# Kernel tuning notes

Measured on AMD Instinct MI355X. Metric: run time of the kernel, lower is better.

The kernel has to match this reference:

```python
import jax, jax.numpy as jnp
import numpy as np

N_HEADS = 8
EMBED_DIM = 64  # per-head dim


def setup_inputs() -> dict:
    key = jax.random.key(0)
    k1, k2, k3 = jax.random.split(key, 3)
    B, S, F = 2, 2048, 512
    x = jax.random.normal(k1, (B, S, F), dtype=jnp.float32)
    W = jax.random.normal(k2, (F, EMBED_DIM * N_HEADS * 3), dtype=jnp.float32) * 0.02
    b = jax.random.normal(k3, (EMBED_DIM * N_HEADS * 3,), dtype=jnp.float32) * 0.02
    return {"x": x, "W": W, "b": b}


def reference(x, W, b):
    B, S, F = x.shape
    H, E = N_HEADS, EMBED_DIM
    emb = x @ W + b                                   # (B, S, E*H*3)
    heads = emb.reshape(B, S, E, H, 3)
    heads = jnp.transpose(heads, (0, 4, 3, 1, 2))     # (B, 3, H, S, E)
    q, k, v = heads[:, 0], heads[:, 1], heads[:, 2]   # each (B, H, S, E)
    qk = jnp.einsum('bhse,bhte->bhst', q, k)          # (B, H, S, S)
    # Original multiplies softmax by `scaling` then divides by it -> exact cancel.
    # Note: no scaling applied BEFORE softmax in the source (faithful).
    attn = jax.nn.softmax(qk, axis=-1)
    out = jnp.einsum('bhst,bhte->bhse', attn, v)      # (B, H, S, E)
    out = jnp.transpose(out, (0, 2, 1, 3)).reshape(B, S, H * E)
    return out
```

## Files before the change

kernel.cpp:

```cpp
#include <hip/hip_runtime.h>


using half8  = __attribute__((ext_vector_type(8))) _Float16;
using f32x4  = __attribute__((ext_vector_type(4))) float;
using float4v = __attribute__((ext_vector_type(4))) float;
using uint2v = __attribute__((ext_vector_type(2))) unsigned int;
using uint4v = __attribute__((ext_vector_type(4))) unsigned int;

constexpr int BN = 2, HN = 8, SN = 2048, EN = 64, FN = 512;
constexpr size_t T_ELEMS = (size_t)BN * HN * SN * EN;

constexpr size_t WB_BYTES = (size_t)24 * 16 * 4 * 64 * 8 * 2;
constexpr size_t BP_OFF   = WB_BYTES;
constexpr size_t X16_OFF  = BP_OFF + 1536 * 4;
constexpr size_t X16_BYTES = (size_t)4096 * 512 * 2;
constexpr size_t QKV_OFF  = X16_OFF + X16_BYTES;

__device__ inline unsigned int pack2h(float a, float b) {
  auto h = __builtin_amdgcn_cvt_pkrtz(a, b);
  return __builtin_bit_cast(unsigned int, h);
}

__device__ __forceinline__ void async_copy16(void* lds, const void* g) {
  __builtin_amdgcn_global_load_lds(
      (const __attribute__((address_space(1))) unsigned int*)g,
      (__attribute__((address_space(3))) unsigned int*)lds, 16, 0, 0);
}

__global__ __launch_bounds__(256) void repack_kernel(
    const float* __restrict__ W, const float* __restrict__ bias,
    _Float16* __restrict__ Wb, float* __restrict__ bp) {
  int t = blockIdx.x * 256 + threadIdx.x;
  int lane = t & 63;
  int cb = (t >> 6) & 3;
  int kc = (t >> 8) & 15;
  int ch = t >> 12;
  int e = cb * 16 + (lane & 15);
  int fb = kc * 32 + (lane >> 4) * 8;
  int c = ch >> 3, h = ch & 7;
  int j = e * 24 + h * 3 + c;
  half8 o;
  #pragma unroll
  for (int i = 0; i < 8; ++i) o[i] = (_Float16)W[(size_t)(fb + i) * 1536 + j];
  *(half8*)(Wb + (size_t)t * 8) = o;
  if (t < 1536) {
    int cc = t % 3, hh = (t / 3) & 7, ee = t / 24;
    bp[(cc * 8 + hh) * 64 + ee] = bias[t];
  }
}

__global__ __launch_bounds__(256) void x16_kernel(const float* __restrict__ x,
                                                  _Float16* __restrict__ x16) {
  int t = blockIdx.x * 256 + threadIdx.x;
  const float4v* src = (const float4v*)(x + (size_t)t * 8);
  float4v a = src[0], b = src[1];
  half8 o;
  #pragma unroll
  for (int i = 0; i < 4; ++i) { o[i] = (_Float16)a[i]; o[4 + i] = (_Float16)b[i]; }
  *(half8*)(x16 + (size_t)t * 8) = o;
}

__global__ __launch_bounds__(256) void proj_kernel(
    const _Float16* __restrict__ x16, const _Float16* __restrict__ Wb,
    const float* __restrict__ bp, _Float16* __restrict__ qkv) {
  int rt = blockIdx.x, cg = blockIdx.y;
  int wave = threadIdx.x >> 6, lane = threadIdx.x & 63;
  int lcol = lane & 15, lg = lane >> 4;
  int row0 = rt * 64 + wave * 16;
  f32x4 acc[3][4] = {};
  const _Float16* xr = x16 + (size_t)(row0 + lcol) * FN;
  for (int kc = 0; kc < 16; ++kc) {
    half8 a = *(const half8*)(xr + kc * 32 + lg * 8);
    #pragma unroll
    for (int chi = 0; chi < 3; ++chi) {
      int ch = cg * 3 + chi;
      #pragma unroll
      for (int cb = 0; cb < 4; ++cb) {
        half8 bfr = *(const half8*)(Wb + ((((size_t)ch * 16 + kc) * 4 + cb) * 64 + lane) * 8);
        acc[chi][cb] = __builtin_amdgcn_mfma_f32_16x16x32_f16(a, bfr, acc[chi][cb], 0, 0, 0);
      }
    }
  }
  #pragma unroll
  for (int chi = 0; chi < 3; ++chi) {
    int ch = cg * 3 + chi;
    int c = ch >> 3, h = ch & 7;
    _Float16* dst = qkv + (size_t)c * T_ELEMS;
    #pragma unroll
    for (int cb = 0; cb < 4; ++cb) {
      int e = cb * 16 + lcol;
      float bv = bp[ch * 64 + e];
      #pragma unroll
      for (int r = 0; r < 4; ++r) {
        int grow = row0 + lg * 4 + r;
        int b = grow >> 11, s = grow & 2047;
        dst[((size_t)(b * HN + h) * SN + s) * EN + e] = (_Float16)(acc[chi][cb][r] + bv);
      }
    }
  }
}

__global__ __launch_bounds__(256) void vtrans_kernel(const _Float16* __restrict__ v,
                                                     _Float16* __restrict__ vt) {
  __shared__ _Float16 tl[64 * 65];
  int bh = blockIdx.x >> 5, st = blockIdx.x & 31;
  int t = threadIdx.x;
  int s0 = st * 64;
  int sl = t >> 3, e0 = (t & 7) * 8;
  #pragma unroll
  for (int rr = 0; rr < 2; ++rr) {
    half8 vv = *(const half8*)(v + ((size_t)bh * SN + s0 + sl + rr * 32) * EN + e0);
    #pragma unroll
    for (int i = 0; i < 8; ++i) tl[(sl + rr * 32) * 65 + e0 + i] = vv[i];
  }
  __syncthreads();
  int e = t >> 2, sc = t & 3;
  half8 o0, o1;
  #pragma unroll
  for (int i = 0; i < 8; ++i) o0[i] = tl[(sc * 16 + i) * 65 + e];
  #pragma unroll
  for (int i = 0; i < 8; ++i) o1[i] = tl[(sc * 16 + 8 + i) * 65 + e];
  _Float16* dst = vt + ((size_t)bh * EN + e) * SN + s0 + sc * 16;
  *(half8*)dst = o0;
  *(half8*)(dst + 8) = o1;
}

__global__ __launch_bounds__(256, 2) void attn_kernel(
    const _Float16* __restrict__ q_ws, const _Float16* __restrict__ k_ws,
    const _Float16* __restrict__ vt_ws, float* __restrict__ out) {
  __shared__ __align__(16) char smem[40960];

  int bid = blockIdx.x;
  int lb = (bid & 7) * 64 + (bid >> 3);
  int bh = lb >> 5, qblk = lb & 31;
  int wave = threadIdx.x >> 6, lane = threadIdx.x & 63;
  int q = lane & 15, g = lane >> 4;
  int q0 = qblk * 64 + wave * 16;

  const _Float16* qb  = q_ws  + ((size_t)bh * SN + q0) * EN;
  const _Float16* kb  = k_ws  + (size_t)bh * SN * EN;
  const _Float16* vtb = vt_ws + (size_t)bh * EN * SN;

  half8 qf[2];
  qf[0] = *(const half8*)(qb + (size_t)q * EN + g * 8);
  qf[1] = *(const half8*)(qb + (size_t)q * EN + 32 + g * 8);

  f32x4 o[4] = {};
  float m = -3e38f, l = 0.f;
  unsigned int* pw = (unsigned int*)(smem + 32768 + wave * 2048);

  int sub = lane >> 3;
  int off8 = ((lane & 7) ^ sub) * 8;
  int lin = lane * 16;

  auto stage = [&](int c, int t) {
    char* kbuf = smem + c * 16384;
    char* vbuf = kbuf + 8192;
    int kv = t * 64;
    #pragma unroll
    for (int ii = 0; ii < 2; ++ii) {
      int i = wave * 2 + ii;
      int row = i * 8 + sub;
      async_copy16(kbuf + i * 1024 + lin, kb + (size_t)(kv + row) * EN + off8);
      async_copy16(vbuf + i * 1024 + lin, vtb + (size_t)row * SN + kv + off8);
    }
  };

  stage(0, 0);
  asm volatile("s_waitcnt vmcnt(0)" ::: "memory");
  __syncthreads();

  int qx = (q & 7) << 4;
  for (int t = 0; t < 32; ++t) {
    int c = t & 1;
    if (t + 1 < 32) stage(c ^ 1, t + 1);
    const char* kbuf = smem + c * 16384;
    const char* vbuf = kbuf + 8192;

    half8 kf[4][2], vf[4][2];
    #pragma unroll
    for (int kt = 0; kt < 4; ++kt)
      #pragma unroll
      for (int eh = 0; eh < 2; ++eh)
        kf[kt][eh] = *(const half8*)(kbuf + ((((kt * 16 + q) * 128) + eh * 64 + g * 16) ^ qx));
    #pragma unroll
    for (int et = 0; et < 4; ++et)
      #pragma unroll
      for (int kh = 0; kh < 2; ++kh)
        vf[et][kh] = *(const half8*)(vbuf + ((((et * 16 + q) * 128) + kh * 64 + g * 16) ^ qx));

    f32x4 s[4];
    f32x4 z = {};
    __builtin_amdgcn_s_setprio(1);
    #pragma unroll
    for (int kt = 0; kt < 4; ++kt) {
      s[kt] = __builtin_amdgcn_mfma_f32_16x16x32_f16(kf[kt][0], qf[0], z, 0, 0, 0);
      s[kt] = __builtin_amdgcn_mfma_f32_16x16x32_f16(kf[kt][1], qf[1], s[kt], 0, 0, 0);
    }
    __builtin_amdgcn_s_setprio(0);

    float mx = s[0][0];
    #pragma unroll
    for (int kt = 0; kt < 4; ++kt)
      #pragma unroll
      for (int r = 0; r < 4; ++r) mx = fmaxf(mx, s[kt][r]);
    mx = fmaxf(mx, __shfl_xor(mx, 16));
    mx = fmaxf(mx, __shfl_xor(mx, 32));
    if (!__all(mx <= m + 8.f)) {
      float mn = fmaxf(m, mx);
      float scl = __expf(m - mn);
      m = mn;
      l *= scl;
      #pragma unroll
      for (int et = 0; et < 4; ++et)
        #pragma unroll
        for (int r = 0; r < 4; ++r) o[et][r] *= scl;
    }
    float ps = 0.f;
    #pragma unroll
    for (int kt = 0; kt < 4; ++kt) {
      float p0 = __expf(s[kt][0] - m), p1 = __expf(s[kt][1] - m);
      float p2 = __expf(s[kt][2] - m), p3 = __expf(s[kt][3] - m);
      ps += (p0 + p1) + (p2 + p3);
      uint2v wv;
      wv.x = pack2h(p0, p1);
      wv.y = pack2h(p2, p3);
      int w = kt * 8 + 2 * g;
      int phys = (((w >> 2) + q) & 7) * 4 + (w & 3);
      *(uint2v*)&pw[q * 32 + phys] = wv;
    }
    l += ps;
    asm volatile("s_waitcnt lgkmcnt(0)" ::: "memory");
    __builtin_amdgcn_sched_barrier(0);
    half8 pf[2];
    #pragma unroll
    for (int kh = 0; kh < 2; ++kh) {
      int cc = kh * 4 + g;
      uint4v tv = *(const uint4v*)&pw[q * 32 + ((cc + q) & 7) * 4];
      pf[kh] = __builtin_bit_cast(half8, tv);
    }
    __builtin_amdgcn_sched_barrier(0);
    __builtin_amdgcn_s_setprio(1);
    #pragma unroll
    for (int et = 0; et < 4; ++et) {
      o[et] = __builtin_amdgcn_mfma_f32_16x16x32_f16(vf[et][0], pf[0], o[et], 0, 0, 0);
      o[et] = __builtin_amdgcn_mfma_f32_16x16x32_f16(vf[et][1], pf[1], o[et], 0, 0, 0);
    }
    __builtin_amdgcn_s_setprio(0);

    asm volatile("s_waitcnt vmcnt(0)" ::: "memory");
    __syncthreads();
  }

  l += __shfl_xor(l, 16);
  l += __shfl_xor(l, 32);
  float rl = 1.f / l;
  int b = bh >> 3, h = bh & 7;
  float* ow = (float*)(smem + wave * 4096);
  #pragma unroll
  for (int et = 0; et < 4; ++et)
    #pragma unroll
    for (int r = 0; r < 4; ++r) {
      int e = et * 16 + g * 4 + r;
      ow[q * 64 + ((e + q * 4) & 63)] = o[et][r] * rl;
    }
  asm volatile("s_waitcnt lgkmcnt(0)" ::: "memory");
  __builtin_amdgcn_sched_barrier(0);
  #pragma unroll
  for (int qr = 0; qr < 16; ++qr) {
    float vvv = ow[qr * 64 + ((lane + qr * 4) & 63)];
    out[((size_t)b * SN + q0 + qr) * 512 + h * 64 + lane] = vvv;
  }
}

extern "C" void kernel_launch(void* const* d_in, const int* in_sizes, int n_in,
                              void* d_out, int out_size, void* d_ws, size_t ws_size,
                              hipStream_t stream) {
  const float* x    = (const float*)d_in[0];
  const float* W    = (const float*)d_in[1];
  const float* bias = (const float*)d_in[2];
  float* out = (float*)d_out;
  char* ws = (char*)d_ws;
  _Float16* Wb  = (_Float16*)(ws);
  float*    bp  = (float*)(ws + BP_OFF);
  _Float16* x16 = (_Float16*)(ws + X16_OFF);
  _Float16* qkv = (_Float16*)(ws + QKV_OFF);
  _Float16* vt  = (_Float16*)(ws + X16_OFF);

  repack_kernel<<<384, 256, 0, stream>>>(W, bias, Wb, bp);
  x16_kernel<<<1024, 256, 0, stream>>>(x, x16);
  proj_kernel<<<dim3(64, 8), 256, 0, stream>>>(x16, Wb, bp, qkv);
  vtrans_kernel<<<512, 256, 0, stream>>>(qkv + 2 * T_ELEMS, vt);
  attn_kernel<<<512, 256, 0, stream>>>(qkv, qkv + T_ELEMS, vt, out);
}
```

Baseline: 130.9 us.

## Fuse x conversion and V transpose into projection; triple-buffer attention K/V

The separate fp32→fp16 conversion kernel for x is removed; the projection kernel now loads fp32 x and converts in registers. The V transpose kernel is also folded into the projection epilogue, which transposes V through shared memory and writes Vt directly. The attention kernel moves from double to triple buffering of K/V tiles, issuing loads two tiles ahead with a partial vmcnt wait, which raises LDS use to 56KB per block. Together these remove two kernel launches and their extra global round-trips, and deepen the load prefetch, at the cost of larger fp32 reads in projection and more LDS pressure in attention.

```diff
diff --git a/kernel.cpp b/kernel.cpp
--- a/kernel.cpp
+++ b/kernel.cpp
@@ -12,9 +12,9 @@
 
 constexpr size_t WB_BYTES = (size_t)24 * 16 * 4 * 64 * 8 * 2;
 constexpr size_t BP_OFF   = WB_BYTES;
-constexpr size_t X16_OFF  = BP_OFF + 1536 * 4;
-constexpr size_t X16_BYTES = (size_t)4096 * 512 * 2;
-constexpr size_t QKV_OFF  = X16_OFF + X16_BYTES;
+constexpr size_t VT_OFF   = BP_OFF + 1536 * 4;
+constexpr size_t VT_BYTES = T_ELEMS * 2;
+constexpr size_t QKV_OFF  = VT_OFF + VT_BYTES;
 
 __device__ inline unsigned int pack2h(float a, float b) {
   auto h = __builtin_amdgcn_cvt_pkrtz(a, b);
@@ -49,28 +49,23 @@
   }
 }
 
-__global__ __launch_bounds__(256) void x16_kernel(const float* __restrict__ x,
-                                                  _Float16* __restrict__ x16) {
-  int t = blockIdx.x * 256 + threadIdx.x;
-  const float4v* src = (const float4v*)(x + (size_t)t * 8);
-  float4v a = src[0], b = src[1];
-  half8 o;
-  #pragma unroll
-  for (int i = 0; i < 4; ++i) { o[i] = (_Float16)a[i]; o[4 + i] = (_Float16)b[i]; }
-  *(half8*)(x16 + (size_t)t * 8) = o;
-}
-
 __global__ __launch_bounds__(256) void proj_kernel(
-    const _Float16* __restrict__ x16, const _Float16* __restrict__ Wb,
-    const float* __restrict__ bp, _Float16* __restrict__ qkv) {
+    const float* __restrict__ x, const _Float16* __restrict__ Wb,
+    const float* __restrict__ bp, _Float16* __restrict__ qkv,
+    _Float16* __restrict__ vt) {
+  __shared__ _Float16 tl[64 * 72];
   int rt = blockIdx.x, cg = blockIdx.y;
   int wave = threadIdx.x >> 6, lane = threadIdx.x & 63;
   int lcol = lane & 15, lg = lane >> 4;
   int row0 = rt * 64 + wave * 16;
   f32x4 acc[3][4] = {};
-  const _Float16* xr = x16 + (size_t)(row0 + lcol) * FN;
+  const float* xr = x + (size_t)(row0 + lcol) * FN;
   for (int kc = 0; kc < 16; ++kc) {
-    half8 a = *(const half8*)(xr + kc * 32 + lg * 8);
+    const float4v* xp = (const float4v*)(xr + kc * 32 + lg * 8);
+    float4v x0 = xp[0], x1 = xp[1];
+    half8 a;
+    #pragma unroll
+    for (int i = 0; i < 4; ++i) { a[i] = (_Float16)x0[i]; a[4 + i] = (_Float16)x1[i]; }
     #pragma unroll
     for (int chi = 0; chi < 3; ++chi) {
       int ch = cg * 3 + chi;
@@ -81,54 +76,51 @@
       }
     }
   }
+  int b = rt >> 5, s0 = (rt & 31) * 64;
   #pragma unroll
   for (int chi = 0; chi < 3; ++chi) {
     int ch = cg * 3 + chi;
     int c = ch >> 3, h = ch & 7;
-    _Float16* dst = qkv + (size_t)c * T_ELEMS;
-    #pragma unroll
-    for (int cb = 0; cb < 4; ++cb) {
-      int e = cb * 16 + lcol;
-      float bv = bp[ch * 64 + e];
-      #pragma unroll
-      for (int r = 0; r < 4; ++r) {
-        int grow = row0 + lg * 4 + r;
-        int b = grow >> 11, s = grow & 2047;
-        dst[((size_t)(b * HN + h) * SN + s) * EN + e] = (_Float16)(acc[chi][cb][r] + bv);
+    if (c < 2) {
+      _Float16* dst = qkv + (size_t)c * T_ELEMS;
+      #pragma unroll
+      for (int cb = 0; cb < 4; ++cb) {
+        int e = cb * 16 + lcol;
+        float bv = bp[ch * 64 + e];
+        #pragma unroll
+        for (int r = 0; r < 4; ++r) {
+          int s = s0 + wave * 16 + lg * 4 + r;
+          dst[((size_t)(b * HN + h) * SN + s) * EN + e] = (_Float16)(acc[chi][cb][r] + bv);
+        }
       }
-    }
-  }
-}
-
-__global__ __launch_bounds__(256) void vtrans_kernel(const _Float16* __restrict__ v,
-                                                     _Float16* __restrict__ vt) {
-  __shared__ _Float16 tl[64 * 65];
-  int bh = blockIdx.x >> 5, st = blockIdx.x & 31;
-  int t = threadIdx.x;
-  int s0 = st * 64;
-  int sl = t >> 3, e0 = (t & 7) * 8;
-  #pragma unroll
-  for (int rr = 0; rr < 2; ++rr) {
-    half8 vv = *(const half8*)(v + ((size_t)bh * SN + s0 + sl + rr * 32) * EN + e0);
-    #pragma unroll
-    for (int i = 0; i < 8; ++i) tl[(sl + rr * 32) * 65 + e0 + i] = vv[i];
-  }
-  __syncthreads();
-  int e = t >> 2, sc = t & 3;
-  half8 o0, o1;
-  #pragma unroll
-  for (int i = 0; i < 8; ++i) o0[i] = tl[(sc * 16 + i) * 65 + e];
-  #pragma unroll
-  for (int i = 0; i < 8; ++i) o1[i] = tl[(sc * 16 + 8 + i) * 65 + e];
-  _Float16* dst = vt + ((size_t)bh * EN + e) * SN + s0 + sc * 16;
-  *(half8*)dst = o0;
-  *(half8*)(dst + 8) = o1;
+    } else {
+      #pragma unroll
+      for (int cb = 0; cb < 4; ++cb) {
+        int e = cb * 16 + lcol;
+        float bv = bp[ch * 64 + e];
+        #pragma unroll
+        for (int r = 0; r < 4; ++r)
+          tl[(wave * 16 + lg * 4 + r) * 72 + e] = (_Float16)(acc[chi][cb][r] + bv);
+      }
+      __syncthreads();
+      int e = threadIdx.x >> 2, sc = threadIdx.x & 3;
+      half8 o0, o1;
+      #pragma unroll
+      for (int i = 0; i < 8; ++i) o0[i] = tl[(sc * 16 + i) * 72 + e];
+      #pragma unroll
+      for (int i = 0; i < 8; ++i) o1[i] = tl[(sc * 16 + 8 + i) * 72 + e];
+      _Float16* dstv = vt + ((size_t)(b * HN + h) * EN + e) * SN + s0 + sc * 16;
+      *(half8*)dstv = o0;
+      *(half8*)(dstv + 8) = o1;
+      __syncthreads();
+    }
+  }
 }
 
 __global__ __launch_bounds__(256, 2) void attn_kernel(
     const _Float16* __restrict__ q_ws, const _Float16* __restrict__ k_ws,
     const _Float16* __restrict__ vt_ws, float* __restrict__ out) {
-  __shared__ __align__(16) char smem[40960];
+  __shared__ __align__(16) char smem[57344];
 
   int bid = blockIdx.x;
   int lb = (bid & 7) * 64 + (bid >> 3);
@@ -147,7 +139,7 @@
 
   f32x4 o[4] = {};
   float m = -3e38f, l = 0.f;
-  unsigned int* pw = (unsigned int*)(smem + 32768 + wave * 2048);
+  unsigned int* pw = (unsigned int*)(smem + 49152 + wave * 2048);
 
   int sub = lane >> 3;
   int off8 = ((lane & 7) ^ sub) * 8;
@@ -166,17 +158,11 @@
     }
   };
 
-  stage(0, 0);
-  asm volatile("s_waitcnt vmcnt(0)" ::: "memory");
-  __syncthreads();
-
   int qx = (q & 7) << 4;
-  for (int t = 0; t < 32; ++t) {
-    int c = t & 1;
-    if (t + 1 < 32) stage(c ^ 1, t + 1);
+
+  auto compute = [&](int c) {
     const char* kbuf = smem + c * 16384;
     const char* vbuf = kbuf + 8192;
-
     half8 kf[4][2], vf[4][2];
     #pragma unroll
     for (int kt = 0; kt < 4; ++kt)
@@ -247,10 +233,19 @@
       o[et] = __builtin_amdgcn_mfma_f32_16x16x32_f16(vf[et][1], pf[1], o[et], 0, 0, 0);
     }
     __builtin_amdgcn_s_setprio(0);
-
-    asm volatile("s_waitcnt vmcnt(0)" ::: "memory");
+  };
+
+  stage(0, 0);
+  stage(1, 1);
+  for (int t = 0; t < 31; ++t) {
+    asm volatile("s_waitcnt vmcnt(4)" ::: "memory");
     __syncthreads();
-  }
+    if (t + 2 < 32) stage((t + 2) % 3, t + 2);
+    compute(t % 3);
+  }
+  asm volatile("s_waitcnt vmcnt(0)" ::: "memory");
+  __syncthreads();
+  compute(31 % 3);
 
   l += __shfl_xor(l, 16);
   l += __shfl_xor(l, 32);
@@ -283,13 +278,10 @@
   char* ws = (char*)d_ws;
   _Float16* Wb  = (_Float16*)(ws);
   float*    bp  = (float*)(ws + BP_OFF);
-  _Float16* x16 = (_Float16*)(ws + X16_OFF);
+  _Float16* vt  = (_Float16*)(ws + VT_OFF);
   _Float16* qkv = (_Float16*)(ws + QKV_OFF);
-  _Float16* vt  = (_Float16*)(ws + X16_OFF);
 
   repack_kernel<<<384, 256, 0, stream>>>(W, bias, Wb, bp);
-  x16_kernel<<<1024, 256, 0, stream>>>(x, x16);
-  proj_kernel<<<dim3(64, 8), 256, 0, stream>>>(x16, Wb, bp, qkv);
-  vtrans_kernel<<<512, 256, 0, stream>>>(qkv + 2 * T_ELEMS, vt);
+  proj_kernel<<<dim3(64, 8), 256, 0, stream>>>(x, Wb, bp, qkv, vt);
   attn_kernel<<<512, 256, 0, stream>>>(qkv, qkv + T_ELEMS, vt, out);
 }
```

Measured after the change: 133.4 us. No clear change (+1.9%).
